# Kernel tuning notes

Measured on AMD Instinct MI355X. Metric: run time of the kernel, lower is better.

## Reference

```python
import jax, jax.numpy as jnp
import numpy as np

K = 64  # key_features
V = 64  # value_features


def setup_inputs() -> dict:
    key = jax.random.key(0)
    ks = jax.random.split(key, 7)
    B, IN, M = 512, 512, 2048
    H = 2 * K + V  # 192, hidden_state dim == output dim of layer
    return {
        "x": jax.random.normal(ks[0], (B, IN), dtype=jnp.float32),
        "hidden_state": jax.random.normal(ks[1], (B, H), dtype=jnp.float32),
        "content": jax.random.normal(ks[2], (B, V), dtype=jnp.float32),
        "key_mem": jax.random.normal(ks[3], (B, K, M), dtype=jnp.float32),
        "value_mem": jax.random.normal(ks[4], (B, V, M), dtype=jnp.float32),
        "W": jax.random.normal(ks[5], (H, IN + 2 * K + 2 * V), dtype=jnp.float32) * 0.02,
        "b": jax.random.normal(ks[6], (H,), dtype=jnp.float32) * 0.02,
    }


def reference(x, hidden_state, content, key_mem, value_mem, W, b):
    # dropout in eval mode (identity); relu on hidden_state
    inp = jnp.concatenate([x, jax.nn.relu(hidden_state), content], axis=1)  # [B, IN+2K+2V]
    o = inp @ W.T + b  # [B, 2K+V]
    query = o[:, :K]            # [B, K]
    # buffer.read: attention over memory slots
    scores = jnp.einsum("bkm,bk->bm", key_mem, query)   # [B, M]
    attn = jax.nn.softmax(scores, axis=1)               # [B, M]
    content_new = jnp.einsum("bvm,bm->bv", value_mem, attn)  # [B, V]
    # buffer.write (state update, returned for completeness of math; original
    # mutates buffer in place; key @ II is exactly a right-shift by one slot):
    new_key = o[:, K:2 * K]
    new_value = o[:, 2 * K:2 * K + V]
    key_mem_next = jnp.concatenate([new_key[:, :, None], key_mem[:, :, :-1]], axis=2)
    value_mem_next = jnp.concatenate([new_value[:, :, None], value_mem[:, :, :-1]], axis=2)
    del key_mem_next, value_mem_next  # forward output matches original: (o, content)
    return (o, content_new)
```

## Files before the change

kernel.cpp:

```cpp
#include <hip/hip_runtime.h>

#define KDIM 64
#define VDIM 64
#define MDIM 2048
#define BDIM 512
#define INDIM 512
#define HDIM 192
#define CIN 768
#define O_SIZE (BDIM*HDIM)

__global__ __launch_bounds__(512, 4)
void memlinear_kernel(const float* __restrict__ x,
                      const float* __restrict__ hidden,
                      const float* __restrict__ content,
                      const float* __restrict__ key_mem,
                      const float* __restrict__ value_mem,
                      const float* __restrict__ W,
                      const float* __restrict__ bias,
                      float* __restrict__ out)
{
    const int b    = blockIdx.x;
    const int tid  = threadIdx.x;
    const int lane = tid & 63;
    const int wid  = tid >> 6;

    __shared__ __align__(16) float inp[CIN];
    __shared__ float q[KDIM];
    __shared__ float red[8];
    __shared__ __align__(16) float attn_lds[MDIM];

    if (tid < INDIM) inp[tid] = x[(size_t)b*INDIM + tid];
    if (tid < HDIM)  inp[INDIM + tid] = fmaxf(hidden[(size_t)b*HDIM + tid], 0.f);
    if (tid < VDIM)  inp[INDIM + HDIM + tid] = content[(size_t)b*VDIM + tid];
    __syncthreads();

    if (tid < 2*HDIM) {
        const int j    = tid >> 1;
        const int half = tid & 1;
        const float4* w4 = reinterpret_cast<const float4*>(W)
                           + (size_t)j * (CIN/4) + half * (CIN/8);
        const float4* i4 = reinterpret_cast<const float4*>(inp) + half * (CIN/8);
        float ax = 0.f, ay = 0.f, az = 0.f, aw = 0.f;
        #pragma unroll
        for (int r = 0; r < CIN/8; r += 8) {
            float4 wr[8];
            #pragma unroll
            for (int u = 0; u < 8; ++u) wr[u] = w4[r + u];
            #pragma unroll
            for (int u = 0; u < 8; ++u) {
                float4 v = i4[r + u];
                ax = fmaf(wr[u].x, v.x, ax);
                ay = fmaf(wr[u].y, v.y, ay);
                az = fmaf(wr[u].z, v.z, az);
                aw = fmaf(wr[u].w, v.w, aw);
            }
        }
        float p = (ax + ay) + (az + aw);
        p += __shfl_xor(p, 1);
        if (half == 0) {
            float o = p + bias[j];
            out[(size_t)b*HDIM + j] = o;
            if (j < KDIM) q[j] = o;
        }
    }
    __syncthreads();

    const float4* km4 = reinterpret_cast<const float4*>(key_mem + (size_t)b*KDIM*MDIM);
    float4 s = make_float4(0.f, 0.f, 0.f, 0.f);
    #pragma unroll
    for (int k0 = 0; k0 < KDIM; k0 += 8) {
        float4 kk[8];
        #pragma unroll
        for (int u = 0; u < 8; ++u)
            kk[u] = km4[(size_t)(k0 + u) * (MDIM/4) + tid];
        #pragma unroll
        for (int u = 0; u < 8; ++u) {
            float qk = q[k0 + u];
            s.x = fmaf(qk, kk[u].x, s.x);
            s.y = fmaf(qk, kk[u].y, s.y);
            s.z = fmaf(qk, kk[u].z, s.z);
            s.w = fmaf(qk, kk[u].w, s.w);
        }
    }

    float mx = fmaxf(fmaxf(s.x, s.y), fmaxf(s.z, s.w));
    #pragma unroll
    for (int off = 32; off >= 1; off >>= 1)
        mx = fmaxf(mx, __shfl_xor(mx, off));
    if (lane == 0) red[wid] = mx;
    __syncthreads();
    float m_all = red[0];
    #pragma unroll
    for (int w = 1; w < 8; ++w) m_all = fmaxf(m_all, red[w]);

    float4 e;
    e.x = __expf(s.x - m_all);
    e.y = __expf(s.y - m_all);
    e.z = __expf(s.z - m_all);
    e.w = __expf(s.w - m_all);
    float sum = (e.x + e.y) + (e.z + e.w);
    #pragma unroll
    for (int off = 32; off >= 1; off >>= 1)
        sum += __shfl_xor(sum, off);
    __syncthreads();
    if (lane == 0) red[wid] = sum;
    __syncthreads();
    float total = 0.f;
    #pragma unroll
    for (int w = 0; w < 8; ++w) total += red[w];
    float inv = 1.0f / total;

    reinterpret_cast<float4*>(attn_lds)[tid] =
        make_float4(e.x*inv, e.y*inv, e.z*inv, e.w*inv);
    __syncthreads();

    const float4* a4 = reinterpret_cast<const float4*>(attn_lds);
    float4 aa[8];
    #pragma unroll
    for (int i = 0; i < 8; ++i) aa[i] = a4[i*64 + lane];

    const float4* vm4 = reinterpret_cast<const float4*>(value_mem + (size_t)b*VDIM*MDIM);
    #pragma unroll
    for (int vi = 0; vi < 8; ++vi) {
        int v = wid*8 + vi;
        float4 vv[8];
        #pragma unroll
        for (int i = 0; i < 8; ++i)
            vv[i] = vm4[(size_t)v*(MDIM/4) + i*64 + lane];
        float px = 0.f, py = 0.f, pz = 0.f, pw = 0.f;
        #pragma unroll
        for (int i = 0; i < 8; ++i) {
            px = fmaf(vv[i].x, aa[i].x, px);
            py = fmaf(vv[i].y, aa[i].y, py);
            pz = fmaf(vv[i].z, aa[i].z, pz);
            pw = fmaf(vv[i].w, aa[i].w, pw);
        }
        float p = (px + py) + (pz + pw);
        #pragma unroll
        for (int off = 32; off >= 1; off >>= 1)
            p += __shfl_xor(p, off);
        if (lane == 0) out[O_SIZE + (size_t)b*VDIM + v] = p;
    }
}

extern "C" void kernel_launch(void* const* d_in, const int* in_sizes, int n_in,
                              void* d_out, int out_size, void* d_ws, size_t ws_size,
                              hipStream_t stream) {
    const float* x         = (const float*)d_in[0];
    const float* hidden    = (const float*)d_in[1];
    const float* content   = (const float*)d_in[2];
    const float* key_mem   = (const float*)d_in[3];
    const float* value_mem = (const float*)d_in[4];
    const float* W         = (const float*)d_in[5];
    const float* bias      = (const float*)d_in[6];
    float* out = (float*)d_out;

    memlinear_kernel<<<dim3(BDIM), dim3(512), 0, stream>>>(
        x, hidden, content, key_mem, value_mem, W, bias, out);
}
```

Baseline: 138.8 us.

## Split fused memory-attention kernel into four kernels with finer-grained parallelism

Replaces the single per-batch fused kernel with four launches: linear projection, scores over key memory split into four slot chunks per batch, a separate softmax pass over a workspace buffer, and a value reduction with one wavefront per (batch, value) pair. The aim is more blocks in flight and better latency hiding on the memory-bound key/value reads, which dominate traffic (about 512 MB in total). The cost is extra launch overhead, a round trip of the scores through global workspace, and the linear step now using only 192 threads per block.

```diff
diff --git a/kernel.cpp b/kernel.cpp
--- a/kernel.cpp
+++ b/kernel.cpp
@@ -9,40 +9,27 @@
 #define CIN 768
 #define O_SIZE (BDIM*HDIM)
 
-__global__ __launch_bounds__(512, 4)
-void memlinear_kernel(const float* __restrict__ x,
-                      const float* __restrict__ hidden,
-                      const float* __restrict__ content,
-                      const float* __restrict__ key_mem,
-                      const float* __restrict__ value_mem,
-                      const float* __restrict__ W,
-                      const float* __restrict__ bias,
-                      float* __restrict__ out)
+__global__ __launch_bounds__(256)
+void gemm_kernel(const float* __restrict__ x, const float* __restrict__ hidden,
+                 const float* __restrict__ content, const float* __restrict__ W,
+                 const float* __restrict__ bias, float* __restrict__ out)
 {
-    const int b    = blockIdx.x;
-    const int tid  = threadIdx.x;
-    const int lane = tid & 63;
-    const int wid  = tid >> 6;
+    const int b   = blockIdx.x;
+    const int tid = threadIdx.x;
+    __shared__ __align__(16) float inp[CIN];
 
-    __shared__ __align__(16) float inp[CIN];
-    __shared__ float q[KDIM];
-    __shared__ float red[8];
-    __shared__ __align__(16) float attn_lds[MDIM];
-
-    if (tid < INDIM) inp[tid] = x[(size_t)b*INDIM + tid];
-    if (tid < HDIM)  inp[INDIM + tid] = fmaxf(hidden[(size_t)b*HDIM + tid], 0.f);
-    if (tid < VDIM)  inp[INDIM + HDIM + tid] = content[(size_t)b*VDIM + tid];
+    inp[tid]       = x[(size_t)b*INDIM + tid];
+    inp[256 + tid] = x[(size_t)b*INDIM + 256 + tid];
+    if (tid < HDIM) inp[INDIM + tid] = fmaxf(hidden[(size_t)b*HDIM + tid], 0.f);
+    if (tid < VDIM) inp[INDIM + HDIM + tid] = content[(size_t)b*VDIM + tid];
     __syncthreads();
 
-    if (tid < 2*HDIM) {
-        const int j    = tid >> 1;
-        const int half = tid & 1;
-        const float4* w4 = reinterpret_cast<const float4*>(W)
-                           + (size_t)j * (CIN/4) + half * (CIN/8);
-        const float4* i4 = reinterpret_cast<const float4*>(inp) + half * (CIN/8);
+    if (tid < HDIM) {
+        const float4* w4 = reinterpret_cast<const float4*>(W) + (size_t)tid * (CIN/4);
+        const float4* i4 = reinterpret_cast<const float4*>(inp);
         float ax = 0.f, ay = 0.f, az = 0.f, aw = 0.f;
         #pragma unroll
-        for (int r = 0; r < CIN/8; r += 8) {
+        for (int r = 0; r < CIN/4; r += 8) {
             float4 wr[8];
             #pragma unroll
             for (int u = 0; u < 8; ++u) wr[u] = w4[r + u];
@@ -55,92 +42,118 @@
                 aw = fmaf(wr[u].w, v.w, aw);
             }
         }
-        float p = (ax + ay) + (az + aw);
-        p += __shfl_xor(p, 1);
-        if (half == 0) {
-            float o = p + bias[j];
-            out[(size_t)b*HDIM + j] = o;
-            if (j < KDIM) q[j] = o;
-        }
+        out[(size_t)b*HDIM + tid] = (ax + ay) + (az + aw) + bias[tid];
     }
+}
+
+__global__ __launch_bounds__(256, 8)
+void scores_kernel(const float* __restrict__ key_mem,
+                   const float* __restrict__ o,
+                   float* __restrict__ scores)
+{
+    const int bid  = blockIdx.x;
+    const int b    = bid >> 2;
+    const int mb   = (bid & 3) * 512;
+    const int tid  = threadIdx.x;
+
+    __shared__ float q[KDIM];
+    if (tid < KDIM) q[tid] = o[(size_t)b*HDIM + tid];
     __syncthreads();
 
-    const float4* km4 = reinterpret_cast<const float4*>(key_mem + (size_t)b*KDIM*MDIM);
-    float4 s = make_float4(0.f, 0.f, 0.f, 0.f);
+    const float2* km2 = reinterpret_cast<const float2*>(key_mem)
+                        + ((size_t)b*KDIM*MDIM + mb)/2 + tid;
+    float sx = 0.f, sy = 0.f;
     #pragma unroll
     for (int k0 = 0; k0 < KDIM; k0 += 8) {
-        float4 kk[8];
+        float2 kk[8];
         #pragma unroll
         for (int u = 0; u < 8; ++u)
-            kk[u] = km4[(size_t)(k0 + u) * (MDIM/4) + tid];
+            kk[u] = km2[(size_t)(k0 + u) * (MDIM/2)];
         #pragma unroll
         for (int u = 0; u < 8; ++u) {
             float qk = q[k0 + u];
-            s.x = fmaf(qk, kk[u].x, s.x);
-            s.y = fmaf(qk, kk[u].y, s.y);
-            s.z = fmaf(qk, kk[u].z, s.z);
-            s.w = fmaf(qk, kk[u].w, s.w);
+            sx = fmaf(qk, kk[u].x, sx);
+            sy = fmaf(qk, kk[u].y, sy);
         }
     }
+    reinterpret_cast<float2*>(scores)[(size_t)b*(MDIM/2) + mb/2 + tid]
+        = make_float2(sx, sy);
+}
 
-    float mx = fmaxf(fmaxf(s.x, s.y), fmaxf(s.z, s.w));
+__global__ __launch_bounds__(256)
+void softmax_kernel(float* __restrict__ scores)
+{
+    const int b    = blockIdx.x;
+    const int tid  = threadIdx.x;
+    const int lane = tid & 63;
+    const int wid  = tid >> 6;
+    __shared__ float red[4];
+
+    float4* row4 = reinterpret_cast<float4*>(scores + (size_t)b*MDIM);
+    float4 s0 = row4[tid];
+    float4 s1 = row4[256 + tid];
+
+    float mx = fmaxf(fmaxf(fmaxf(s0.x, s0.y), fmaxf(s0.z, s0.w)),
+                     fmaxf(fmaxf(s1.x, s1.y), fmaxf(s1.z, s1.w)));
     #pragma unroll
-    for (int off = 32; off >= 1; off >>= 1)
-        mx = fmaxf(mx, __shfl_xor(mx, off));
+    for (int off = 32; off >= 1; off >>= 1) mx = fmaxf(mx, __shfl_xor(mx, off));
     if (lane == 0) red[wid] = mx;
     __syncthreads();
-    float m_all = red[0];
+    float m_all = fmaxf(fmaxf(red[0], red[1]), fmaxf(red[2], red[3]));
+
+    float4 e0, e1;
+    e0.x = __expf(s0.x - m_all); e0.y = __expf(s0.y - m_all);
+    e0.z = __expf(s0.z - m_all); e0.w = __expf(s0.w - m_all);
+    e1.x = __expf(s1.x - m_all); e1.y = __expf(s1.y - m_all);
+    e1.z = __expf(s1.z - m_all); e1.w = __expf(s1.w - m_all);
+    float sum = (e0.x + e0.y) + (e0.z + e0.w) + (e1.x + e1.y) + (e1.z + e1.w);
     #pragma unroll
-    for (int w = 1; w < 8; ++w) m_all = fmaxf(m_all, red[w]);
-
-    float4 e;
-    e.x = __expf(s.x - m_all);
-    e.y = __expf(s.y - m_all);
-    e.z = __expf(s.z - m_all);
-    e.w = __expf(s.w - m_all);
-    float sum = (e.x + e.y) + (e.z + e.w);
-    #pragma unroll
-    for (int off = 32; off >= 1; off >>= 1)
-        sum += __shfl_xor(sum, off);
+    for (int off = 32; off >= 1; off >>= 1) sum += __shfl_xor(sum, off);
     __syncthreads();
     if (lane == 0) red[wid] = sum;
     __syncthreads();
-    float total = 0.f;
+    float inv = 1.0f / (red[0] + red[1] + red[2] + red[3]);
+
+    e0.x *= inv; e0.y *= inv; e0.z *= inv; e0.w *= inv;
+    e1.x *= inv; e1.y *= inv; e1.z *= inv; e1.w *= inv;
+    row4[tid]       = e0;
+    row4[256 + tid] = e1;
+}
+
+__global__ __launch_bounds__(256, 4)
+void pv_kernel(const float* __restrict__ value_mem,
+               const float* __restrict__ attn,
+               float* __restrict__ out)
+{
+    const int tid  = threadIdx.x;
+    const int lane = tid & 63;
+    const int wid  = tid >> 6;
+    const int gwid = blockIdx.x * 4 + wid;
+    const int b    = gwid >> 6;
+    const int v    = gwid & 63;
+
+    const float4* vm4 = reinterpret_cast<const float4*>(value_mem)
+                        + ((size_t)b*VDIM + v) * (MDIM/4);
+    const float4* a4  = reinterpret_cast<const float4*>(attn) + (size_t)b*(MDIM/4);
+
+    float4 vv[8], aa[8];
     #pragma unroll
-    for (int w = 0; w < 8; ++w) total += red[w];
-    float inv = 1.0f / total;
-
-    reinterpret_cast<float4*>(attn_lds)[tid] =
-        make_float4(e.x*inv, e.y*inv, e.z*inv, e.w*inv);
-    __syncthreads();
-
-    const float4* a4 = reinterpret_cast<const float4*>(attn_lds);
-    float4 aa[8];
+    for (int i = 0; i < 8; ++i) vv[i] = vm4[i*64 + lane];
     #pragma unroll
     for (int i = 0; i < 8; ++i) aa[i] = a4[i*64 + lane];
 
-    const float4* vm4 = reinterpret_cast<const float4*>(value_mem + (size_t)b*VDIM*MDIM);
+    float px = 0.f, py = 0.f, pz = 0.f, pw = 0.f;
     #pragma unroll
-    for (int vi = 0; vi < 8; ++vi) {
-        int v = wid*8 + vi;
-        float4 vv[8];
-        #pragma unroll
-        for (int i = 0; i < 8; ++i)
-            vv[i] = vm4[(size_t)v*(MDIM/4) + i*64 + lane];
-        float px = 0.f, py = 0.f, pz = 0.f, pw = 0.f;
-        #pragma unroll
-        for (int i = 0; i < 8; ++i) {
-            px = fmaf(vv[i].x, aa[i].x, px);
-            py = fmaf(vv[i].y, aa[i].y, py);
-            pz = fmaf(vv[i].z, aa[i].z, pz);
-            pw = fmaf(vv[i].w, aa[i].w, pw);
-        }
-        float p = (px + py) + (pz + pw);
-        #pragma unroll
-        for (int off = 32; off >= 1; off >>= 1)
-            p += __shfl_xor(p, off);
-        if (lane == 0) out[O_SIZE + (size_t)b*VDIM + v] = p;
+    for (int i = 0; i < 8; ++i) {
+        px = fmaf(vv[i].x, aa[i].x, px);
+        py = fmaf(vv[i].y, aa[i].y, py);
+        pz = fmaf(vv[i].z, aa[i].z, pz);
+        pw = fmaf(vv[i].w, aa[i].w, pw);
     }
+    float p = (px + py) + (pz + pw);
+    #pragma unroll
+    for (int off = 32; off >= 1; off >>= 1) p += __shfl_xor(p, off);
+    if (lane == 0) out[O_SIZE + (size_t)b*VDIM + v] = p;
 }
 
 extern "C" void kernel_launch(void* const* d_in, const int* in_sizes, int n_in,
@@ -153,8 +166,11 @@
     const float* value_mem = (const float*)d_in[4];
     const float* W         = (const float*)d_in[5];
     const float* bias      = (const float*)d_in[6];
-    float* out = (float*)d_out;
+    float* out    = (float*)d_out;
+    float* scores = (float*)d_ws;
 
-    memlinear_kernel<<<dim3(BDIM), dim3(512), 0, stream>>>(
-        x, hidden, content, key_mem, value_mem, W, bias, out);
+    gemm_kernel   <<<dim3(BDIM),        dim3(256), 0, stream>>>(x, hidden, content, W, bias, out);
+    scores_kernel <<<dim3(BDIM*4),      dim3(256), 0, stream>>>(key_mem, out, scores);
+    softmax_kernel<<<dim3(BDIM),        dim3(256), 0, stream>>>(scores);
+    pv_kernel     <<<dim3(BDIM*VDIM/4), dim3(256), 0, stream>>>(value_mem, scores, out);
 }
```

After: 149.7 us. 7.8% more time.

## Split fused kernel into GEMM and attention kernels with 1024-thread attention blocks

Applied to the files above, without the earlier changes.

The single fused kernel becomes two launches. The first computes the linear layer o. The second reads the query from o and runs the memory attention with 1024 threads per batch row, each thread handling two slots (float2) instead of four. Splitting is meant to keep the GEMM phase from stalling the bandwidth-bound key/value memory streaming and to give more waves in flight. The cost is an extra launch, o making a round trip through global memory, and narrower key loads.

```diff
diff --git a/kernel.cpp b/kernel.cpp
--- a/kernel.cpp
+++ b/kernel.cpp
@@ -9,29 +9,18 @@
 #define CIN 768
 #define O_SIZE (BDIM*HDIM)
 
-__global__ __launch_bounds__(512, 4)
-void memlinear_kernel(const float* __restrict__ x,
-                      const float* __restrict__ hidden,
-                      const float* __restrict__ content,
-                      const float* __restrict__ key_mem,
-                      const float* __restrict__ value_mem,
-                      const float* __restrict__ W,
-                      const float* __restrict__ bias,
-                      float* __restrict__ out)
+__global__ __launch_bounds__(512)
+void gemm_kernel(const float* __restrict__ x, const float* __restrict__ hidden,
+                 const float* __restrict__ content, const float* __restrict__ W,
+                 const float* __restrict__ bias, float* __restrict__ out)
 {
-    const int b    = blockIdx.x;
-    const int tid  = threadIdx.x;
-    const int lane = tid & 63;
-    const int wid  = tid >> 6;
+    const int b   = blockIdx.x;
+    const int tid = threadIdx.x;
+    __shared__ __align__(16) float inp[CIN];
 
-    __shared__ __align__(16) float inp[CIN];
-    __shared__ float q[KDIM];
-    __shared__ float red[8];
-    __shared__ __align__(16) float attn_lds[MDIM];
-
-    if (tid < INDIM) inp[tid] = x[(size_t)b*INDIM + tid];
-    if (tid < HDIM)  inp[INDIM + tid] = fmaxf(hidden[(size_t)b*HDIM + tid], 0.f);
-    if (tid < VDIM)  inp[INDIM + HDIM + tid] = content[(size_t)b*VDIM + tid];
+    inp[tid] = x[(size_t)b*INDIM + tid];
+    if (tid < HDIM) inp[INDIM + tid] = fmaxf(hidden[(size_t)b*HDIM + tid], 0.f);
+    if (tid < VDIM) inp[INDIM + HDIM + tid] = content[(size_t)b*VDIM + tid];
     __syncthreads();
 
     if (tid < 2*HDIM) {
@@ -57,72 +46,76 @@
         }
         float p = (ax + ay) + (az + aw);
         p += __shfl_xor(p, 1);
-        if (half == 0) {
-            float o = p + bias[j];
-            out[(size_t)b*HDIM + j] = o;
-            if (j < KDIM) q[j] = o;
-        }
+        if (half == 0) out[(size_t)b*HDIM + j] = p + bias[j];
     }
+}
+
+__global__ __launch_bounds__(1024, 8)
+void attn_kernel(const float* __restrict__ key_mem,
+                 const float* __restrict__ value_mem,
+                 const float* __restrict__ o,
+                 float* __restrict__ out)
+{
+    const int b    = blockIdx.x;
+    const int tid  = threadIdx.x;
+    const int lane = tid & 63;
+    const int wid  = tid >> 6;
+
+    __shared__ float q[KDIM];
+    __shared__ float red[16];
+    __shared__ __align__(16) float attn_lds[MDIM];
+
+    if (tid < KDIM) q[tid] = o[(size_t)b*HDIM + tid];
     __syncthreads();
 
-    const float4* km4 = reinterpret_cast<const float4*>(key_mem + (size_t)b*KDIM*MDIM);
-    float4 s = make_float4(0.f, 0.f, 0.f, 0.f);
+    const float2* km2 = reinterpret_cast<const float2*>(key_mem)
+                        + (size_t)b * KDIM * (MDIM/2) + tid;
+    float sx = 0.f, sy = 0.f;
     #pragma unroll
     for (int k0 = 0; k0 < KDIM; k0 += 8) {
-        float4 kk[8];
+        float2 kk[8];
         #pragma unroll
         for (int u = 0; u < 8; ++u)
-            kk[u] = km4[(size_t)(k0 + u) * (MDIM/4) + tid];
+            kk[u] = km2[(size_t)(k0 + u) * (MDIM/2)];
         #pragma unroll
         for (int u = 0; u < 8; ++u) {
             float qk = q[k0 + u];
-            s.x = fmaf(qk, kk[u].x, s.x);
-            s.y = fmaf(qk, kk[u].y, s.y);
-            s.z = fmaf(qk, kk[u].z, s.z);
-            s.w = fmaf(qk, kk[u].w, s.w);
+            sx = fmaf(qk, kk[u].x, sx);
+            sy = fmaf(qk, kk[u].y, sy);
         }
     }
 
-    float mx = fmaxf(fmaxf(s.x, s.y), fmaxf(s.z, s.w));
+    float mx = fmaxf(sx, sy);
     #pragma unroll
-    for (int off = 32; off >= 1; off >>= 1)
-        mx = fmaxf(mx, __shfl_xor(mx, off));
+    for (int off = 32; off >= 1; off >>= 1) mx = fmaxf(mx, __shfl_xor(mx, off));
     if (lane == 0) red[wid] = mx;
     __syncthreads();
     float m_all = red[0];
     #pragma unroll
-    for (int w = 1; w < 8; ++w) m_all = fmaxf(m_all, red[w]);
+    for (int w = 1; w < 16; ++w) m_all = fmaxf(m_all, red[w]);
 
-    float4 e;
-    e.x = __expf(s.x - m_all);
-    e.y = __expf(s.y - m_all);
-    e.z = __expf(s.z - m_all);
-    e.w = __expf(s.w - m_all);
-    float sum = (e.x + e.y) + (e.z + e.w);
+    float ex = __expf(sx - m_all);
+    float ey = __expf(sy - m_all);
+    float sum = ex + ey;
     #pragma unroll
-    for (int off = 32; off >= 1; off >>= 1)
-        sum += __shfl_xor(sum, off);
+    for (int off = 32; off >= 1; off >>= 1) sum += __shfl_xor(sum, off);
     __syncthreads();
     if (lane == 0) red[wid] = sum;
     __syncthreads();
     float total = 0.f;
     #pragma unroll
-    for (int w = 0; w < 8; ++w) total += red[w];
+    for (int w = 0; w < 16; ++w) total += red[w];
     float inv = 1.0f / total;
 
-    reinterpret_cast<float4*>(attn_lds)[tid] =
-        make_float4(e.x*inv, e.y*inv, e.z*inv, e.w*inv);
+    reinterpret_cast<float2*>(attn_lds)[tid] = make_float2(ex*inv, ey*inv);
     __syncthreads();
 
-    const float4* a4 = reinterpret_cast<const float4*>(attn_lds);
-    float4 aa[8];
+    const float4* vm4 = reinterpret_cast<const float4*>(value_mem)
+                        + (size_t)b * VDIM * (MDIM/4);
+    const float4* a4  = reinterpret_cast<const float4*>(attn_lds);
     #pragma unroll
-    for (int i = 0; i < 8; ++i) aa[i] = a4[i*64 + lane];
-
-    const float4* vm4 = reinterpret_cast<const float4*>(value_mem + (size_t)b*VDIM*MDIM);
-    #pragma unroll
-    for (int vi = 0; vi < 8; ++vi) {
-        int v = wid*8 + vi;
+    for (int vi = 0; vi < 4; ++vi) {
+        const int v = wid*4 + vi;
         float4 vv[8];
         #pragma unroll
         for (int i = 0; i < 8; ++i)
@@ -130,15 +123,15 @@
         float px = 0.f, py = 0.f, pz = 0.f, pw = 0.f;
         #pragma unroll
         for (int i = 0; i < 8; ++i) {
-            px = fmaf(vv[i].x, aa[i].x, px);
-            py = fmaf(vv[i].y, aa[i].y, py);
-            pz = fmaf(vv[i].z, aa[i].z, pz);
-            pw = fmaf(vv[i].w, aa[i].w, pw);
+            float4 aa = a4[i*64 + lane];
+            px = fmaf(vv[i].x, aa.x, px);
+            py = fmaf(vv[i].y, aa.y, py);
+            pz = fmaf(vv[i].z, aa.z, pz);
+            pw = fmaf(vv[i].w, aa.w, pw);
         }
         float p = (px + py) + (pz + pw);
         #pragma unroll
-        for (int off = 32; off >= 1; off >>= 1)
-            p += __shfl_xor(p, off);
+        for (int off = 32; off >= 1; off >>= 1) p += __shfl_xor(p, off);
         if (lane == 0) out[O_SIZE + (size_t)b*VDIM + v] = p;
     }
 }
@@ -155,6 +148,6 @@
     const float* bias      = (const float*)d_in[6];
     float* out = (float*)d_out;
 
-    memlinear_kernel<<<dim3(BDIM), dim3(512), 0, stream>>>(
-        x, hidden, content, key_mem, value_mem, W, bias, out);
+    gemm_kernel<<<dim3(BDIM), dim3(512),  0, stream>>>(x, hidden, content, W, bias, out);
+    attn_kernel<<<dim3(BDIM), dim3(1024), 0, stream>>>(key_mem, value_mem, out, out);
 }
```

After: 151.5 us. 9.2% more time.
